# Performance work log

Hardware: AMD Instinct MI355X
Metric: run time of the kernel (lower is better)

The kernel has to match this reference:

```python
import jax, jax.numpy as jnp
import numpy as np

B, P_DIM, H_DIM, X_DIM = 4096, 1024, 2048, 1024


def setup_inputs() -> dict:
    key = jax.random.key(0)
    ks = jax.random.split(key, 24)
    def lin_w(k, out_d, in_d):
        bound = 1.0 / np.sqrt(in_d)
        return jax.random.uniform(k, (out_d, in_d), jnp.float32, -bound, bound)
    def lin_b(k, out_d, in_d):
        bound = 1.0 / np.sqrt(in_d)
        return jax.random.uniform(k, (out_d,), jnp.float32, -bound, bound)
    inp = {
        "P": jax.random.normal(ks[0], (B, P_DIM), jnp.float32),
        "hidden": jax.random.normal(ks[1], (B, H_DIM), jnp.float32),
        "cell": jax.random.normal(ks[2], (B, H_DIM), jnp.float32),
        "ext_input": jax.random.normal(ks[3], (B, X_DIM), jnp.float32),
        "W_pi": lin_w(ks[4], H_DIM, P_DIM), "b_pi": lin_b(ks[5], H_DIM, P_DIM),
        "W_pf": lin_w(ks[6], H_DIM, P_DIM), "b_pf": lin_b(ks[7], H_DIM, P_DIM),
        "W_pg": lin_w(ks[8], H_DIM, P_DIM), "b_pg": lin_b(ks[9], H_DIM, P_DIM),
        "W_po": lin_w(ks[10], H_DIM, P_DIM), "b_po": lin_b(ks[11], H_DIM, P_DIM),
        "W_hi": lin_w(ks[12], H_DIM, H_DIM), "W_hf": lin_w(ks[13], H_DIM, H_DIM),
        "W_hg": lin_w(ks[14], H_DIM, H_DIM), "W_ho": lin_w(ks[15], H_DIM, H_DIM),
        "W_xi": lin_w(ks[16], H_DIM, X_DIM), "W_xf": lin_w(ks[17], H_DIM, X_DIM),
        "W_xg": lin_w(ks[18], H_DIM, X_DIM), "W_xo": lin_w(ks[19], H_DIM, X_DIM),
    }
    return inp


def reference(P, hidden, cell, ext_input,
              W_pi, b_pi, W_pf, b_pf, W_pg, b_pg, W_po, b_po,
              W_hi, W_hf, W_hg, W_ho,
              W_xi, W_xf, W_xg, W_xo):
    # Concatenate the 4 per-gate weights along the output axis -> 3 big GEMMs
    # (mathematically identical to the 12 separate nn.Linear calls).
    Wp = jnp.concatenate([W_pi, W_pf, W_pg, W_po], axis=0)   # [4H, P]
    bp = jnp.concatenate([b_pi, b_pf, b_pg, b_po], axis=0)   # [4H]
    Wh = jnp.concatenate([W_hi, W_hf, W_hg, W_ho], axis=0)   # [4H, H]
    Wx = jnp.concatenate([W_xi, W_xf, W_xg, W_xo], axis=0)   # [4H, X]
    gates = P @ Wp.T + bp + hidden @ Wh.T + ext_input @ Wx.T  # [B, 4H]
    gi, gf, gg, go = jnp.split(gates, 4, axis=-1)
    i = jax.nn.sigmoid(gi)
    f = jax.nn.sigmoid(gf)
    g = jnp.tanh(gg)
    o = jax.nn.sigmoid(go)
    c_new = f * cell + i * g
    h_new = o * jnp.tanh(c_new)
    return (h_new, c_new)
```

## Files before the change

### kernel.cpp

```cpp
#include <hip/hip_runtime.h>
#include <hip/hip_bf16.h>
#include <stdint.h>

#define B_DIM 4096
#define P_DIMC 1024
#define H_DIMC 2048
#define X_DIMC 1024
#define K_DIM 4096
#define N_DIM 8192

#define BM 256
#define BN 256
#define BK 64
#define NT (K_DIM / BK)

typedef __attribute__((ext_vector_type(8))) short bf16x8;
typedef __attribute__((ext_vector_type(4))) float f32x4;

template <int V> struct Int { static constexpr int value = V; };

__device__ __forceinline__ unsigned short f2bf(float f) {
  union { float f; unsigned u; } v; v.f = f;
  unsigned u = v.u;
  u += 0x7FFFu + ((u >> 16) & 1u);
  return (unsigned short)(u >> 16);
}

__device__ __forceinline__ float sigm(float x) { return 1.f / (1.f + __expf(-x)); }
__device__ __forceinline__ float tanh_fast(float x) {
  float e = __expf(2.f * x);
  return 1.f - 2.f / (e + 1.f);
}

__device__ __forceinline__ void gl_lds16(const void* g, void* l) {
  __builtin_amdgcn_global_load_lds((const __attribute__((address_space(1))) void*)g,
                                   (__attribute__((address_space(3))) void*)l, 16, 0, 0);
}

struct WPtrs {
  const float *pi, *pf, *pg, *po;
  const float *hi, *hf, *hg, *ho;
  const float *xi, *xf, *xg, *xo;
};

__global__ void pack_kernel(const float* __restrict__ P, const float* __restrict__ Hd,
                            const float* __restrict__ X, WPtrs w,
                            unsigned short* __restrict__ A, unsigned short* __restrict__ Wo) {
  const int NA = B_DIM * (K_DIM / 8);
  const int NW = N_DIM * (K_DIM / 8);
  for (int idx = blockIdx.x * blockDim.x + threadIdx.x; idx < NA + NW;
       idx += gridDim.x * blockDim.x) {
    const float* src; int off; unsigned short* dst; size_t doff;
    if (idx < NA) {
      int row = idx >> 9;
      int col = (idx & 511) << 3;
      if (col < P_DIMC)                { src = P;  off = row * P_DIMC + col; }
      else if (col < P_DIMC + H_DIMC)  { src = Hd; off = row * H_DIMC + (col - P_DIMC); }
      else                             { src = X;  off = row * X_DIMC + (col - P_DIMC - H_DIMC); }
      dst = A; doff = (size_t)row * K_DIM + col;
    } else {
      int j = idx - NA;
      int n = j >> 9;
      int col = (j & 511) << 3;
      int gate = (n >> 4) & 3;
      int h = ((n >> 6) << 4) | (n & 15);
      if (col < P_DIMC) {
        src = gate == 0 ? w.pi : gate == 1 ? w.pf : gate == 2 ? w.pg : w.po;
        off = h * P_DIMC + col;
      } else if (col < P_DIMC + H_DIMC) {
        src = gate == 0 ? w.hi : gate == 1 ? w.hf : gate == 2 ? w.hg : w.ho;
        off = h * H_DIMC + (col - P_DIMC);
      } else {
        src = gate == 0 ? w.xi : gate == 1 ? w.xf : gate == 2 ? w.xg : w.xo;
        off = h * X_DIMC + (col - P_DIMC - H_DIMC);
      }
      dst = Wo; doff = (size_t)n * K_DIM + col;
    }
    float4 v0 = *(const float4*)(src + off);
    float4 v1 = *(const float4*)(src + off + 4);
    ushort4 o0, o1;
    o0.x = f2bf(v0.x); o0.y = f2bf(v0.y); o0.z = f2bf(v0.z); o0.w = f2bf(v0.w);
    o1.x = f2bf(v1.x); o1.y = f2bf(v1.y); o1.z = f2bf(v1.z); o1.w = f2bf(v1.w);
    union { ushort4 h[2]; uint4 u; } pk;
    pk.h[0] = o0; pk.h[1] = o1;
    *(uint4*)(dst + doff) = pk.u;
  }
}

__global__ __launch_bounds__(512, 1) void gemm_lstm_kernel(
    const unsigned short* __restrict__ A, const unsigned short* __restrict__ W,
    const float* __restrict__ cell,
    const float* __restrict__ bpi, const float* __restrict__ bpf,
    const float* __restrict__ bpg, const float* __restrict__ bpo,
    float* __restrict__ out) {
  __shared__ __align__(16) short As[2][BM * BK];
  __shared__ __align__(16) short Bs[2][BN * BK];

  const int T = threadIdx.x;
  const int wave = T >> 6, lane = T & 63;
  const int wm = wave >> 2, wn = wave & 3;

  const int x = blockIdx.x & 7, local = blockIdx.x >> 3;
  const int bm = (x & 1) * 8 + (local >> 3);
  const int bn = (x >> 1) * 8 + (local & 7);

  const int rowS = T >> 3;
  const int cg = ((T & 7) - (rowS & 7)) & 7;
  const unsigned short* aGq[4];
  const unsigned short* bGq[4];
#pragma unroll
  for (int q = 0; q < 4; ++q) {
    aGq[q] = A + (size_t)(bm * BM + q * 64 + rowS) * K_DIM + cg * 8;
    bGq[q] = W + (size_t)(bn * BN + q * 64 + rowS) * K_DIM + cg * 8;
  }
  const int dstOff = T * 8;

#define STAGE_TILE(BUF, KT)                                                   \
  _Pragma("unroll") for (int q = 0; q < 4; ++q)                               \
    gl_lds16(aGq[q] + (KT), &As[BUF][q * 4096] + dstOff);                     \
  _Pragma("unroll") for (int q = 0; q < 4; ++q)                               \
    gl_lds16(bGq[q] + (KT), &Bs[BUF][q * 4096] + dstOff);

  const int lrow = lane & 15, kgrp = lane >> 4;
  int offA[8][2], offB[4][2];
#pragma unroll
  for (int mf = 0; mf < 8; ++mf)
#pragma unroll
    for (int ks = 0; ks < 2; ++ks)
      offA[mf][ks] = (wm * 128 + mf * 16 + lrow) * BK +
                     (((ks * 4 + kgrp) + (lrow & 7)) & 7) * 8;
#pragma unroll
  for (int nf = 0; nf < 4; ++nf)
#pragma unroll
    for (int ks = 0; ks < 2; ++ks)
      offB[nf][ks] = (wn * 64 + nf * 16 + lrow) * BK +
                     (((ks * 4 + kgrp) + (lrow & 7)) & 7) * 8;

  f32x4 acc[8][4] = {};

  STAGE_TILE(0, 0)
  asm volatile("s_waitcnt vmcnt(0)" ::: "memory");
  __builtin_amdgcn_s_barrier();

  auto run_loop = [&](auto firstc) {
    constexpr int F = decltype(firstc)::value;
    constexpr int S = 4 - F;
    for (int t = 0; t < NT; ++t) {
      const int cur = t & 1, nxt = cur ^ 1;
      const short* bufA = &As[cur][0];
      const short* bufB = &Bs[cur][0];
      bf16x8 av[4], bv[4];

#pragma unroll
      for (int j = 0; j < 4; ++j) bv[j] = *(const bf16x8*)(bufB + offB[j][0]);
#pragma unroll
      for (int i = 0; i < 4; ++i) av[i] = *(const bf16x8*)(bufA + offA[F + i][0]);
      if (t < NT - 1) { STAGE_TILE(nxt, (t + 1) * BK) }
      __builtin_amdgcn_s_setprio(1);
#pragma unroll
      for (int mi = 0; mi < 4; ++mi)
#pragma unroll
        for (int ni = 0; ni < 4; ++ni)
          acc[F + mi][ni] =
              __builtin_amdgcn_mfma_f32_16x16x32_bf16(av[mi], bv[ni], acc[F + mi][ni], 0, 0, 0);
      __builtin_amdgcn_s_setprio(0);
      __builtin_amdgcn_sched_barrier(0);

#pragma unroll
      for (int i = 0; i < 4; ++i) av[i] = *(const bf16x8*)(bufA + offA[S + i][0]);
      __builtin_amdgcn_s_setprio(1);
#pragma unroll
      for (int mi = 0; mi < 4; ++mi)
#pragma unroll
        for (int ni = 0; ni < 4; ++ni)
          acc[S + mi][ni] =
              __builtin_amdgcn_mfma_f32_16x16x32_bf16(av[mi], bv[ni], acc[S + mi][ni], 0, 0, 0);
      __builtin_amdgcn_s_setprio(0);
      __builtin_amdgcn_sched_barrier(0);

#pragma unroll
      for (int j = 0; j < 4; ++j) bv[j] = *(const bf16x8*)(bufB + offB[j][1]);
#pragma unroll
      for (int i = 0; i < 4; ++i) av[i] = *(const bf16x8*)(bufA + offA[F + i][1]);
      __builtin_amdgcn_s_setprio(1);
#pragma unroll
      for (int mi = 0; mi < 4; ++mi)
#pragma unroll
        for (int ni = 0; ni < 4; ++ni)
          acc[F + mi][ni] =
              __builtin_amdgcn_mfma_f32_16x16x32_bf16(av[mi], bv[ni], acc[F + mi][ni], 0, 0, 0);
      __builtin_amdgcn_s_setprio(0);
      __builtin_amdgcn_sched_barrier(0);

#pragma unroll
      for (int i = 0; i < 4; ++i) av[i] = *(const bf16x8*)(bufA + offA[S + i][1]);
      __builtin_amdgcn_s_setprio(1);
#pragma unroll
      for (int mi = 0; mi < 4; ++mi)
#pragma unroll
        for (int ni = 0; ni < 4; ++ni)
          acc[S + mi][ni] =
              __builtin_amdgcn_mfma_f32_16x16x32_bf16(av[mi], bv[ni], acc[S + mi][ni], 0, 0, 0);
      __builtin_amdgcn_s_setprio(0);
      __builtin_amdgcn_sched_barrier(0);

      if (t < NT - 1) {
        asm volatile("s_waitcnt vmcnt(0)" ::: "memory");
        __builtin_amdgcn_s_barrier();
      }
    }
  };
  if (wave & 1) run_loop(Int<4>{});
  else          run_loop(Int<0>{});

  const int h = bn * 64 + wn * 16 + lrow;
  const float bi = bpi[h], bf_ = bpf[h], bg = bpg[h], bo = bpo[h];
  const int rbase = bm * BM + wm * 128 + kgrp * 4;
#pragma unroll
  for (int mf = 0; mf < 8; ++mf) {
#pragma unroll
    for (int r = 0; r < 4; ++r) {
      const int brow = rbase + mf * 16 + r;
      float gi = acc[mf][0][r] + bi;
      float gf = acc[mf][1][r] + bf_;
      float gg = acc[mf][2][r] + bg;
      float go = acc[mf][3][r] + bo;
      float i_ = sigm(gi), f_ = sigm(gf), g_ = tanh_fast(gg), o_ = sigm(go);
      float cold = cell[(size_t)brow * H_DIMC + h];
      float cn = f_ * cold + i_ * g_;
      out[(size_t)brow * H_DIMC + h] = o_ * tanh_fast(cn);
      out[(size_t)B_DIM * H_DIMC + (size_t)brow * H_DIMC + h] = cn;
    }
  }
}

extern "C" void kernel_launch(void* const* d_in, const int* in_sizes, int n_in,
                              void* d_out, int out_size, void* d_ws, size_t ws_size,
                              hipStream_t stream) {
  const float* P    = (const float*)d_in[0];
  const float* Hd   = (const float*)d_in[1];
  const float* cell = (const float*)d_in[2];
  const float* X    = (const float*)d_in[3];
  WPtrs w;
  w.pi = (const float*)d_in[4];   const float* bpi = (const float*)d_in[5];
  w.pf = (const float*)d_in[6];   const float* bpf = (const float*)d_in[7];
  w.pg = (const float*)d_in[8];   const float* bpg = (const float*)d_in[9];
  w.po = (const float*)d_in[10];  const float* bpo = (const float*)d_in[11];
  w.hi = (const float*)d_in[12];  w.hf = (const float*)d_in[13];
  w.hg = (const float*)d_in[14];  w.ho = (const float*)d_in[15];
  w.xi = (const float*)d_in[16];  w.xf = (const float*)d_in[17];
  w.xg = (const float*)d_in[18];  w.xo = (const float*)d_in[19];

  unsigned short* Abf = (unsigned short*)d_ws;
  unsigned short* Wbf = Abf + (size_t)B_DIM * K_DIM;

  pack_kernel<<<2048, 256, 0, stream>>>(P, Hd, X, w, Abf, Wbf);
  gemm_lstm_kernel<<<512, 512, 0, stream>>>(Abf, Wbf, cell, bpi, bpf, bpg, bpo,
                                            (float*)d_out);
}
```

Baseline: 302.6 us.

## Restructure GEMM main loop into half-tile ping-pong pipeline with interleaved weight layout

Splits each LDS buffer into two half-tiles and rewrites the main loop as an eight-phase schedule where each quarter of MFMA work is bracketed by barriers while the next half-tiles stream in, keeping more global loads in flight (vmcnt(6)) instead of draining to zero every K step. The weight permutation and the per-wave row/column mapping change so each wave owns interleaved 16-row/16-column slices, with the epilogue row indexing updated to match. The aim is better overlap of global-to-LDS traffic with matrix math. The cost is many more workgroup barriers per iteration and tighter coupling between waves.

```diff
diff --git a/kernel.cpp b/kernel.cpp
--- a/kernel.cpp
+++ b/kernel.cpp
@@ -62,8 +62,8 @@
       int j = idx - NA;
       int n = j >> 9;
       int col = (j & 511) << 3;
-      int gate = (n >> 4) & 3;
-      int h = ((n >> 6) << 4) | (n & 15);
+      int gate = (n >> 6) & 3;
+      int h = ((n >> 8) << 6) | (n & 63);
       if (col < P_DIMC) {
         src = gate == 0 ? w.pi : gate == 1 ? w.pf : gate == 2 ? w.pg : w.po;
         off = h * P_DIMC + col;
@@ -93,8 +93,8 @@
     const float* __restrict__ bpi, const float* __restrict__ bpf,
     const float* __restrict__ bpg, const float* __restrict__ bpo,
     float* __restrict__ out) {
-  __shared__ __align__(16) short As[2][BM * BK];
-  __shared__ __align__(16) short Bs[2][BN * BK];
+  __shared__ __align__(16) short As[2][2][8192];
+  __shared__ __align__(16) short Bs[2][2][8192];
 
   const int T = threadIdx.x;
   const int wave = T >> 6, lane = T & 63;
@@ -115,116 +115,122 @@
   }
   const int dstOff = T * 8;
 
-#define STAGE_TILE(BUF, KT)                                                   \
-  _Pragma("unroll") for (int q = 0; q < 4; ++q)                               \
-    gl_lds16(aGq[q] + (KT), &As[BUF][q * 4096] + dstOff);                     \
-  _Pragma("unroll") for (int q = 0; q < 4; ++q)                               \
-    gl_lds16(bGq[q] + (KT), &Bs[BUF][q * 4096] + dstOff);
+#define SA(BUF, HALF, KT)                                                     \
+  { gl_lds16(aGq[(HALF)*2] + (KT), &As[BUF][HALF][dstOff]);                   \
+    gl_lds16(aGq[(HALF)*2+1] + (KT), &As[BUF][HALF][4096 + dstOff]); }
+#define SB(BUF, HALF, KT)                                                     \
+  { gl_lds16(bGq[(HALF)*2] + (KT), &Bs[BUF][HALF][dstOff]);                   \
+    gl_lds16(bGq[(HALF)*2+1] + (KT), &Bs[BUF][HALF][4096 + dstOff]); }
 
   const int lrow = lane & 15, kgrp = lane >> 4;
-  int offA[8][2], offB[4][2];
-#pragma unroll
-  for (int mf = 0; mf < 8; ++mf)
+  int sl[2];
+#pragma unroll
+  for (int ks = 0; ks < 2; ++ks) sl[ks] = (((ks * 4 + kgrp) + (lrow & 7)) & 7) * 8;
+  int aOff[4][2], bOff[2][2];
+#pragma unroll
+  for (int i = 0; i < 4; ++i)
 #pragma unroll
     for (int ks = 0; ks < 2; ++ks)
-      offA[mf][ks] = (wm * 128 + mf * 16 + lrow) * BK +
-                     (((ks * 4 + kgrp) + (lrow & 7)) & 7) * 8;
-#pragma unroll
-  for (int nf = 0; nf < 4; ++nf)
+      aOff[i][ks] = (i * 32 + wm * 16 + lrow) * 64 + sl[ks];
+#pragma unroll
+  for (int j = 0; j < 2; ++j)
 #pragma unroll
     for (int ks = 0; ks < 2; ++ks)
-      offB[nf][ks] = (wn * 64 + nf * 16 + lrow) * BK +
-                     (((ks * 4 + kgrp) + (lrow & 7)) & 7) * 8;
+      bOff[j][ks] = (j * 64 + wn * 16 + lrow) * 64 + sl[ks];
 
   f32x4 acc[8][4] = {};
-
-  STAGE_TILE(0, 0)
-  asm volatile("s_waitcnt vmcnt(0)" ::: "memory");
-  __builtin_amdgcn_s_barrier();
-
-  auto run_loop = [&](auto firstc) {
-    constexpr int F = decltype(firstc)::value;
-    constexpr int S = 4 - F;
-    for (int t = 0; t < NT; ++t) {
-      const int cur = t & 1, nxt = cur ^ 1;
-      const short* bufA = &As[cur][0];
-      const short* bufB = &Bs[cur][0];
-      bf16x8 av[4], bv[4];
-
-#pragma unroll
-      for (int j = 0; j < 4; ++j) bv[j] = *(const bf16x8*)(bufB + offB[j][0]);
-#pragma unroll
-      for (int i = 0; i < 4; ++i) av[i] = *(const bf16x8*)(bufA + offA[F + i][0]);
-      if (t < NT - 1) { STAGE_TILE(nxt, (t + 1) * BK) }
-      __builtin_amdgcn_s_setprio(1);
-#pragma unroll
-      for (int mi = 0; mi < 4; ++mi)
-#pragma unroll
-        for (int ni = 0; ni < 4; ++ni)
-          acc[F + mi][ni] =
-              __builtin_amdgcn_mfma_f32_16x16x32_bf16(av[mi], bv[ni], acc[F + mi][ni], 0, 0, 0);
-      __builtin_amdgcn_s_setprio(0);
-      __builtin_amdgcn_sched_barrier(0);
-
-#pragma unroll
-      for (int i = 0; i < 4; ++i) av[i] = *(const bf16x8*)(bufA + offA[S + i][0]);
-      __builtin_amdgcn_s_setprio(1);
-#pragma unroll
-      for (int mi = 0; mi < 4; ++mi)
-#pragma unroll
-        for (int ni = 0; ni < 4; ++ni)
-          acc[S + mi][ni] =
-              __builtin_amdgcn_mfma_f32_16x16x32_bf16(av[mi], bv[ni], acc[S + mi][ni], 0, 0, 0);
-      __builtin_amdgcn_s_setprio(0);
-      __builtin_amdgcn_sched_barrier(0);
-
-#pragma unroll
-      for (int j = 0; j < 4; ++j) bv[j] = *(const bf16x8*)(bufB + offB[j][1]);
-#pragma unroll
-      for (int i = 0; i < 4; ++i) av[i] = *(const bf16x8*)(bufA + offA[F + i][1]);
-      __builtin_amdgcn_s_setprio(1);
-#pragma unroll
-      for (int mi = 0; mi < 4; ++mi)
-#pragma unroll
-        for (int ni = 0; ni < 4; ++ni)
-          acc[F + mi][ni] =
-              __builtin_amdgcn_mfma_f32_16x16x32_bf16(av[mi], bv[ni], acc[F + mi][ni], 0, 0, 0);
-      __builtin_amdgcn_s_setprio(0);
-      __builtin_amdgcn_sched_barrier(0);
-
-#pragma unroll
-      for (int i = 0; i < 4; ++i) av[i] = *(const bf16x8*)(bufA + offA[S + i][1]);
-      __builtin_amdgcn_s_setprio(1);
-#pragma unroll
-      for (int mi = 0; mi < 4; ++mi)
-#pragma unroll
-        for (int ni = 0; ni < 4; ++ni)
-          acc[S + mi][ni] =
-              __builtin_amdgcn_mfma_f32_16x16x32_bf16(av[mi], bv[ni], acc[S + mi][ni], 0, 0, 0);
-      __builtin_amdgcn_s_setprio(0);
-      __builtin_amdgcn_sched_barrier(0);
-
-      if (t < NT - 1) {
-        asm volatile("s_waitcnt vmcnt(0)" ::: "memory");
-        __builtin_amdgcn_s_barrier();
-      }
-    }
+  bf16x8 av[4][2], bv[2][2];
+
+#define RDA(BUF, HALF)                                                        \
+  _Pragma("unroll") for (int i = 0; i < 4; ++i) {                             \
+    av[i][0] = *(const bf16x8*)(&As[BUF][HALF][aOff[i][0]]);                  \
+    av[i][1] = *(const bf16x8*)(&As[BUF][HALF][aOff[i][1]]);                  \
+  }
+#define RDB(BUF, HALF)                                                        \
+  _Pragma("unroll") for (int j = 0; j < 2; ++j) {                             \
+    bv[j][0] = *(const bf16x8*)(&Bs[BUF][HALF][bOff[j][0]]);                  \
+    bv[j][1] = *(const bf16x8*)(&Bs[BUF][HALF][bOff[j][1]]);                  \
+  }
+#define FENCE()                                                               \
+  __builtin_amdgcn_s_barrier();                                               \
+  asm volatile("s_waitcnt lgkmcnt(0)" ::: "memory");                          \
+  __builtin_amdgcn_sched_barrier(0);
+#define MM(MH, NH)                                                            \
+  __builtin_amdgcn_s_setprio(1);                                              \
+  _Pragma("unroll") for (int i = 0; i < 4; ++i)                               \
+  _Pragma("unroll") for (int j = 0; j < 2; ++j) {                             \
+    acc[(MH)*4+i][(NH)*2+j] = __builtin_amdgcn_mfma_f32_16x16x32_bf16(        \
+        av[i][0], bv[j][0], acc[(MH)*4+i][(NH)*2+j], 0, 0, 0);                \
+    acc[(MH)*4+i][(NH)*2+j] = __builtin_amdgcn_mfma_f32_16x16x32_bf16(        \
+        av[i][1], bv[j][1], acc[(MH)*4+i][(NH)*2+j], 0, 0, 0);                \
+  }                                                                           \
+  __builtin_amdgcn_s_setprio(0);
+#define BAR() __builtin_amdgcn_s_barrier();
+
+  SA(0, 0, 0) SB(0, 0, 0) SA(0, 1, 0) SB(0, 1, 0)
+  SB(1, 0, BK) SA(1, 1, BK) SB(1, 1, BK)
+  asm volatile("s_waitcnt vmcnt(6)" ::: "memory");
+  BAR()
+
+  auto iter = [&](int t, auto lastc) {
+    constexpr bool LAST = decltype(lastc)::value;
+    const int k1 = (t + 1) * BK, k2 = (t + 2) * BK, k3 = (t + 3) * BK;
+    (void)k2; (void)k3;
+
+    RDA(0, 0) RDB(0, 0)
+    SA(1, 0, k1)
+    FENCE() MM(0, 0) BAR()
+    RDA(0, 1)
+    if constexpr (!LAST) SB(0, 0, k2)
+    FENCE() MM(1, 0) BAR()
+    RDB(0, 1)
+    if constexpr (!LAST) SA(0, 1, k2)
+    FENCE() MM(1, 1) BAR()
+    RDA(0, 0)
+    if constexpr (!LAST) SB(0, 1, k2)
+    FENCE() MM(0, 1)
+    if constexpr (!LAST) { asm volatile("s_waitcnt vmcnt(6)" ::: "memory"); }
+    else                 { asm volatile("s_waitcnt vmcnt(0)" ::: "memory"); }
+    BAR()
+    RDA(1, 0) RDB(1, 0)
+    if constexpr (!LAST) SA(0, 0, k2)
+    FENCE() MM(0, 0) BAR()
+    RDA(1, 1)
+    if constexpr (!LAST) SB(1, 0, k3)
+    FENCE() MM(1, 0) BAR()
+    RDB(1, 1)
+    if constexpr (!LAST) SA(1, 1, k3)
+    FENCE() MM(1, 1) BAR()
+    RDA(1, 0)
+    if constexpr (!LAST) SB(1, 1, k3)
+    FENCE() MM(0, 1)
+    if constexpr (!LAST) { asm volatile("s_waitcnt vmcnt(6)" ::: "memory"); }
+    BAR()
   };
-  if (wave & 1) run_loop(Int<4>{});
-  else          run_loop(Int<0>{});
+
+  for (int t = 0; t < NT - 2; t += 2) iter(t, Int<0>{});
+  iter(NT - 2, Int<1>{});
+
+#undef SA
+#undef SB
+#undef RDA
+#undef RDB
+#undef FENCE
+#undef MM
+#undef BAR
 
   const int h = bn * 64 + wn * 16 + lrow;
   const float bi = bpi[h], bf_ = bpf[h], bg = bpg[h], bo = bpo[h];
-  const int rbase = bm * BM + wm * 128 + kgrp * 4;
-#pragma unroll
-  for (int mf = 0; mf < 8; ++mf) {
+  const int rbase = bm * BM + wm * 16 + kgrp * 4;
+#pragma unroll
+  for (int a = 0; a < 8; ++a) {
 #pragma unroll
     for (int r = 0; r < 4; ++r) {
-      const int brow = rbase + mf * 16 + r;
-      float gi = acc[mf][0][r] + bi;
-      float gf = acc[mf][1][r] + bf_;
-      float gg = acc[mf][2][r] + bg;
-      float go = acc[mf][3][r] + bo;
+      const int brow = rbase + (a >> 2) * 128 + (a & 3) * 32 + r;
+      float gi = acc[a][0][r] + bi;
+      float gf = acc[a][1][r] + bf_;
+      float gg = acc[a][2][r] + bg;
+      float go = acc[a][3][r] + bo;
       float i_ = sigm(gi), f_ = sigm(gf), g_ = tanh_fast(gg), o_ = sigm(go);
       float cold = cell[(size_t)brow * H_DIMC + h];
       float cn = f_ * cold + i_ * g_;
```

Result: slower. 314.9 us (+4.1%).

## Switch GEMM to 32x32x16 MFMA with 4 waves and 128x128 warp tiles

Applied to the files above, without the earlier changes.

Replaces the 16x16x32 MFMA tiling (8 waves, 128x64 per wave) with 32x32x16 MFMA on 4 waves, each computing a 128x128 sub-tile. The weight pack interleave moves to 32-wide gate groups so each wave's four N-fragments line up with the i/f/g/o gates in the epilogue. LDS fragment reads are double-buffered in registers across the k-substeps. The goal is fewer LDS reads per MFMA and higher MFMA efficiency, at the cost of a large accumulator footprint (256 floats per lane) and half as many waves for hiding latency.

```diff
diff --git a/kernel.cpp b/kernel.cpp
--- a/kernel.cpp
+++ b/kernel.cpp
@@ -15,9 +15,7 @@
 #define NT (K_DIM / BK)
 
 typedef __attribute__((ext_vector_type(8))) short bf16x8;
-typedef __attribute__((ext_vector_type(4))) float f32x4;
-
-template <int V> struct Int { static constexpr int value = V; };
+typedef __attribute__((ext_vector_type(16))) float f32x16;
 
 __device__ __forceinline__ unsigned short f2bf(float f) {
   union { float f; unsigned u; } v; v.f = f;
@@ -62,8 +60,8 @@
       int j = idx - NA;
       int n = j >> 9;
       int col = (j & 511) << 3;
-      int gate = (n >> 4) & 3;
-      int h = ((n >> 6) << 4) | (n & 15);
+      int gate = (n >> 5) & 3;
+      int h = (n >> 7) * 32 + (n & 31);
       if (col < P_DIMC) {
         src = gate == 0 ? w.pi : gate == 1 ? w.pf : gate == 2 ? w.pg : w.po;
         off = h * P_DIMC + col;
@@ -87,7 +85,7 @@
   }
 }
 
-__global__ __launch_bounds__(512, 1) void gemm_lstm_kernel(
+__global__ __launch_bounds__(256, 1) void gemm_lstm_kernel(
     const unsigned short* __restrict__ A, const unsigned short* __restrict__ W,
     const float* __restrict__ cell,
     const float* __restrict__ bpi, const float* __restrict__ bpf,
@@ -98,7 +96,8 @@
 
   const int T = threadIdx.x;
   const int wave = T >> 6, lane = T & 63;
-  const int wm = wave >> 2, wn = wave & 3;
+  const int wm = wave >> 1, wn = wave & 1;
+  const int l31 = lane & 31, khalf = lane >> 5;
 
   const int x = blockIdx.x & 7, local = blockIdx.x >> 3;
   const int bm = (x & 1) * 8 + (local >> 3);
@@ -106,125 +105,89 @@
 
   const int rowS = T >> 3;
   const int cg = ((T & 7) - (rowS & 7)) & 7;
-  const unsigned short* aGq[4];
-  const unsigned short* bGq[4];
-#pragma unroll
-  for (int q = 0; q < 4; ++q) {
-    aGq[q] = A + (size_t)(bm * BM + q * 64 + rowS) * K_DIM + cg * 8;
-    bGq[q] = W + (size_t)(bn * BN + q * 64 + rowS) * K_DIM + cg * 8;
-  }
+  const unsigned short* aB = A + (size_t)(bm * BM + rowS) * K_DIM + cg * 8;
+  const unsigned short* bB = W + (size_t)(bn * BN + rowS) * K_DIM + cg * 8;
   const int dstOff = T * 8;
 
 #define STAGE_TILE(BUF, KT)                                                   \
-  _Pragma("unroll") for (int q = 0; q < 4; ++q)                               \
-    gl_lds16(aGq[q] + (KT), &As[BUF][q * 4096] + dstOff);                     \
-  _Pragma("unroll") for (int q = 0; q < 4; ++q)                               \
-    gl_lds16(bGq[q] + (KT), &Bs[BUF][q * 4096] + dstOff);
-
-  const int lrow = lane & 15, kgrp = lane >> 4;
-  int offA[8][2], offB[4][2];
-#pragma unroll
-  for (int mf = 0; mf < 8; ++mf)
-#pragma unroll
-    for (int ks = 0; ks < 2; ++ks)
-      offA[mf][ks] = (wm * 128 + mf * 16 + lrow) * BK +
-                     (((ks * 4 + kgrp) + (lrow & 7)) & 7) * 8;
-#pragma unroll
-  for (int nf = 0; nf < 4; ++nf)
-#pragma unroll
-    for (int ks = 0; ks < 2; ++ks)
-      offB[nf][ks] = (wn * 64 + nf * 16 + lrow) * BK +
-                     (((ks * 4 + kgrp) + (lrow & 7)) & 7) * 8;
-
-  f32x4 acc[8][4] = {};
+  _Pragma("unroll") for (int q = 0; q < 8; ++q)                               \
+    gl_lds16(aB + (size_t)q * 32 * K_DIM + (KT), &As[BUF][q * 2048] + dstOff);\
+  _Pragma("unroll") for (int q = 0; q < 8; ++q)                               \
+    gl_lds16(bB + (size_t)q * 32 * K_DIM + (KT), &Bs[BUF][q * 2048] + dstOff);
+
+  int sl[4];
+#pragma unroll
+  for (int ks = 0; ks < 4; ++ks)
+    sl[ks] = (((ks * 2 + khalf) + (l31 & 7)) & 7) * 8;
+  int offA[4][4], offB[4][4];
+#pragma unroll
+  for (int mf = 0; mf < 4; ++mf)
+#pragma unroll
+    for (int ks = 0; ks < 4; ++ks) {
+      offA[mf][ks] = (wm * 128 + mf * 32 + l31) * BK + sl[ks];
+      offB[mf][ks] = (wn * 128 + mf * 32 + l31) * BK + sl[ks];
+    }
+
+  f32x16 acc[4][4] = {};
+  bf16x8 av[2][4], bv[2][4];
 
   STAGE_TILE(0, 0)
   asm volatile("s_waitcnt vmcnt(0)" ::: "memory");
   __builtin_amdgcn_s_barrier();
 
-  auto run_loop = [&](auto firstc) {
-    constexpr int F = decltype(firstc)::value;
-    constexpr int S = 4 - F;
-    for (int t = 0; t < NT; ++t) {
-      const int cur = t & 1, nxt = cur ^ 1;
-      const short* bufA = &As[cur][0];
-      const short* bufB = &Bs[cur][0];
-      bf16x8 av[4], bv[4];
-
-#pragma unroll
-      for (int j = 0; j < 4; ++j) bv[j] = *(const bf16x8*)(bufB + offB[j][0]);
-#pragma unroll
-      for (int i = 0; i < 4; ++i) av[i] = *(const bf16x8*)(bufA + offA[F + i][0]);
-      if (t < NT - 1) { STAGE_TILE(nxt, (t + 1) * BK) }
+  for (int t = 0; t < NT; ++t) {
+    const int cur = t & 1, nxt = cur ^ 1;
+    const short* bufA = &As[cur][0];
+    const short* bufB = &Bs[cur][0];
+
+    if (t < NT - 1) { STAGE_TILE(nxt, (t + 1) * BK) }
+
+#pragma unroll
+    for (int i = 0; i < 4; ++i) {
+      av[0][i] = *(const bf16x8*)(bufA + offA[i][0]);
+      bv[0][i] = *(const bf16x8*)(bufB + offB[i][0]);
+    }
+    __builtin_amdgcn_sched_barrier(0);
+
+#pragma unroll
+    for (int ks = 0; ks < 4; ++ks) {
+      const int p = ks & 1, pn = p ^ 1;
+      if (ks < 3) {
+#pragma unroll
+        for (int i = 0; i < 4; ++i) {
+          av[pn][i] = *(const bf16x8*)(bufA + offA[i][ks + 1]);
+          bv[pn][i] = *(const bf16x8*)(bufB + offB[i][ks + 1]);
+        }
+      }
       __builtin_amdgcn_s_setprio(1);
 #pragma unroll
       for (int mi = 0; mi < 4; ++mi)
 #pragma unroll
         for (int ni = 0; ni < 4; ++ni)
-          acc[F + mi][ni] =
-              __builtin_amdgcn_mfma_f32_16x16x32_bf16(av[mi], bv[ni], acc[F + mi][ni], 0, 0, 0);
+          acc[mi][ni] = __builtin_amdgcn_mfma_f32_32x32x16_bf16(
+              av[p][mi], bv[p][ni], acc[mi][ni], 0, 0, 0);
       __builtin_amdgcn_s_setprio(0);
       __builtin_amdgcn_sched_barrier(0);
-
-#pragma unroll
-      for (int i = 0; i < 4; ++i) av[i] = *(const bf16x8*)(bufA + offA[S + i][0]);
-      __builtin_amdgcn_s_setprio(1);
-#pragma unroll
-      for (int mi = 0; mi < 4; ++mi)
-#pragma unroll
-        for (int ni = 0; ni < 4; ++ni)
-          acc[S + mi][ni] =
-              __builtin_amdgcn_mfma_f32_16x16x32_bf16(av[mi], bv[ni], acc[S + mi][ni], 0, 0, 0);
-      __builtin_amdgcn_s_setprio(0);
-      __builtin_amdgcn_sched_barrier(0);
-
-#pragma unroll
-      for (int j = 0; j < 4; ++j) bv[j] = *(const bf16x8*)(bufB + offB[j][1]);
-#pragma unroll
-      for (int i = 0; i < 4; ++i) av[i] = *(const bf16x8*)(bufA + offA[F + i][1]);
-      __builtin_amdgcn_s_setprio(1);
-#pragma unroll
-      for (int mi = 0; mi < 4; ++mi)
-#pragma unroll
-        for (int ni = 0; ni < 4; ++ni)
-          acc[F + mi][ni] =
-              __builtin_amdgcn_mfma_f32_16x16x32_bf16(av[mi], bv[ni], acc[F + mi][ni], 0, 0, 0);
-      __builtin_amdgcn_s_setprio(0);
-      __builtin_amdgcn_sched_barrier(0);
-
-#pragma unroll
-      for (int i = 0; i < 4; ++i) av[i] = *(const bf16x8*)(bufA + offA[S + i][1]);
-      __builtin_amdgcn_s_setprio(1);
-#pragma unroll
-      for (int mi = 0; mi < 4; ++mi)
-#pragma unroll
-        for (int ni = 0; ni < 4; ++ni)
-          acc[S + mi][ni] =
-              __builtin_amdgcn_mfma_f32_16x16x32_bf16(av[mi], bv[ni], acc[S + mi][ni], 0, 0, 0);
-      __builtin_amdgcn_s_setprio(0);
-      __builtin_amdgcn_sched_barrier(0);
-
-      if (t < NT - 1) {
-        asm volatile("s_waitcnt vmcnt(0)" ::: "memory");
-        __builtin_amdgcn_s_barrier();
-      }
-    }
-  };
-  if (wave & 1) run_loop(Int<4>{});
-  else          run_loop(Int<0>{});
-
-  const int h = bn * 64 + wn * 16 + lrow;
+    }
+
+    if (t < NT - 1) {
+      asm volatile("s_waitcnt vmcnt(0)" ::: "memory");
+      __builtin_amdgcn_s_barrier();
+    }
+  }
+
+  const int h = bn * 64 + wn * 32 + l31;
   const float bi = bpi[h], bf_ = bpf[h], bg = bpg[h], bo = bpo[h];
-  const int rbase = bm * BM + wm * 128 + kgrp * 4;
-#pragma unroll
-  for (int mf = 0; mf < 8; ++mf) {
-#pragma unroll
-    for (int r = 0; r < 4; ++r) {
-      const int brow = rbase + mf * 16 + r;
-      float gi = acc[mf][0][r] + bi;
-      float gf = acc[mf][1][r] + bf_;
-      float gg = acc[mf][2][r] + bg;
-      float go = acc[mf][3][r] + bo;
+  const int rbase = bm * BM + wm * 128 + khalf * 4;
+#pragma unroll
+  for (int mf = 0; mf < 4; ++mf) {
+#pragma unroll
+    for (int reg = 0; reg < 16; ++reg) {
+      const int brow = rbase + mf * 32 + (reg & 3) + 8 * (reg >> 2);
+      float gi = acc[mf][0][reg] + bi;
+      float gf = acc[mf][1][reg] + bf_;
+      float gg = acc[mf][2][reg] + bg;
+      float go = acc[mf][3][reg] + bo;
       float i_ = sigm(gi), f_ = sigm(gf), g_ = tanh_fast(gg), o_ = sigm(go);
       float cold = cell[(size_t)brow * H_DIMC + h];
       float cn = f_ * cold + i_ * g_;
@@ -255,6 +218,6 @@
   unsigned short* Wbf = Abf + (size_t)B_DIM * K_DIM;
 
   pack_kernel<<<2048, 256, 0, stream>>>(P, Hd, X, w, Abf, Wbf);
-  gemm_lstm_kernel<<<512, 512, 0, stream>>>(Abf, Wbf, cell, bpi, bpf, bpg, bpo,
+  gemm_lstm_kernel<<<512, 256, 0, stream>>>(Abf, Wbf, cell, bpi, bpf, bpg, bpo,
                                             (float*)d_out);
 }
```

Result: slower. 362.8 us (+19.9%).

## Use 4 waves per block with 128x128 per-wave tiles

Applied to the files above, without the earlier changes.

The GEMM block drops from 8 waves to 4. Each wave now computes a 128x128 output tile (8x8 MFMA fragments) instead of 128x64, which doubles register-level reuse of the A fragments and cuts LDS reads per MFMA. Global-to-LDS staging is redistributed so each of the 256 threads issues 8 loads per operand, and the epilogue loops over two gate groups. The cost is 256 accumulator floats per thread, with a risk of register spills, and fewer waves to hide latency.

```diff
diff --git a/kernel.cpp b/kernel.cpp
--- a/kernel.cpp
+++ b/kernel.cpp
@@ -87,7 +87,7 @@
   }
 }
 
-__global__ __launch_bounds__(512, 1) void gemm_lstm_kernel(
+__global__ __launch_bounds__(256, 1) void gemm_lstm_kernel(
     const unsigned short* __restrict__ A, const unsigned short* __restrict__ W,
     const float* __restrict__ cell,
     const float* __restrict__ bpi, const float* __restrict__ bpf,
@@ -98,7 +98,7 @@
 
   const int T = threadIdx.x;
   const int wave = T >> 6, lane = T & 63;
-  const int wm = wave >> 2, wn = wave & 3;
+  const int wm = wave >> 1, wn = wave & 1;
 
   const int x = blockIdx.x & 7, local = blockIdx.x >> 3;
   const int bm = (x & 1) * 8 + (local >> 3);
@@ -106,37 +106,28 @@
 
   const int rowS = T >> 3;
   const int cg = ((T & 7) - (rowS & 7)) & 7;
-  const unsigned short* aGq[4];
-  const unsigned short* bGq[4];
-#pragma unroll
-  for (int q = 0; q < 4; ++q) {
-    aGq[q] = A + (size_t)(bm * BM + q * 64 + rowS) * K_DIM + cg * 8;
-    bGq[q] = W + (size_t)(bn * BN + q * 64 + rowS) * K_DIM + cg * 8;
-  }
+  const unsigned short* aB = A + (size_t)(bm * BM + rowS) * K_DIM + cg * 8;
+  const unsigned short* bB = W + (size_t)(bn * BN + rowS) * K_DIM + cg * 8;
   const int dstOff = T * 8;
 
 #define STAGE_TILE(BUF, KT)                                                   \
-  _Pragma("unroll") for (int q = 0; q < 4; ++q)                               \
-    gl_lds16(aGq[q] + (KT), &As[BUF][q * 4096] + dstOff);                     \
-  _Pragma("unroll") for (int q = 0; q < 4; ++q)                               \
-    gl_lds16(bGq[q] + (KT), &Bs[BUF][q * 4096] + dstOff);
+  _Pragma("unroll") for (int q = 0; q < 8; ++q)                               \
+    gl_lds16(aB + (size_t)q * 32 * K_DIM + (KT), &As[BUF][q * 2048] + dstOff);\
+  _Pragma("unroll") for (int q = 0; q < 8; ++q)                               \
+    gl_lds16(bB + (size_t)q * 32 * K_DIM + (KT), &Bs[BUF][q * 2048] + dstOff);
 
   const int lrow = lane & 15, kgrp = lane >> 4;
-  int offA[8][2], offB[4][2];
+  int offA[8][2], offB[8][2];
 #pragma unroll
   for (int mf = 0; mf < 8; ++mf)
 #pragma unroll
-    for (int ks = 0; ks < 2; ++ks)
-      offA[mf][ks] = (wm * 128 + mf * 16 + lrow) * BK +
-                     (((ks * 4 + kgrp) + (lrow & 7)) & 7) * 8;
-#pragma unroll
-  for (int nf = 0; nf < 4; ++nf)
-#pragma unroll
-    for (int ks = 0; ks < 2; ++ks)
-      offB[nf][ks] = (wn * 64 + nf * 16 + lrow) * BK +
-                     (((ks * 4 + kgrp) + (lrow & 7)) & 7) * 8;
-
-  f32x4 acc[8][4] = {};
+    for (int ks = 0; ks < 2; ++ks) {
+      const int slot = (((ks * 4 + kgrp) + (lrow & 7)) & 7) * 8;
+      offA[mf][ks] = (wm * 128 + mf * 16 + lrow) * BK + slot;
+      offB[mf][ks] = (wn * 128 + mf * 16 + lrow) * BK + slot;
+    }
+
+  f32x4 acc[8][8] = {};
 
   STAGE_TILE(0, 0)
   asm volatile("s_waitcnt vmcnt(0)" ::: "memory");
@@ -149,10 +140,10 @@
       const int cur = t & 1, nxt = cur ^ 1;
       const short* bufA = &As[cur][0];
       const short* bufB = &Bs[cur][0];
-      bf16x8 av[4], bv[4];
-
-#pragma unroll
-      for (int j = 0; j < 4; ++j) bv[j] = *(const bf16x8*)(bufB + offB[j][0]);
+      bf16x8 av[4], bv[8];
+
+#pragma unroll
+      for (int j = 0; j < 8; ++j) bv[j] = *(const bf16x8*)(bufB + offB[j][0]);
 #pragma unroll
       for (int i = 0; i < 4; ++i) av[i] = *(const bf16x8*)(bufA + offA[F + i][0]);
       if (t < NT - 1) { STAGE_TILE(nxt, (t + 1) * BK) }
@@ -160,7 +151,7 @@
 #pragma unroll
       for (int mi = 0; mi < 4; ++mi)
 #pragma unroll
-        for (int ni = 0; ni < 4; ++ni)
+        for (int ni = 0; ni < 8; ++ni)
           acc[F + mi][ni] =
               __builtin_amdgcn_mfma_f32_16x16x32_bf16(av[mi], bv[ni], acc[F + mi][ni], 0, 0, 0);
       __builtin_amdgcn_s_setprio(0);
@@ -172,21 +163,21 @@
 #pragma unroll
       for (int mi = 0; mi < 4; ++mi)
 #pragma unroll
-        for (int ni = 0; ni < 4; ++ni)
+        for (int ni = 0; ni < 8; ++ni)
           acc[S + mi][ni] =
               __builtin_amdgcn_mfma_f32_16x16x32_bf16(av[mi], bv[ni], acc[S + mi][ni], 0, 0, 0);
       __builtin_amdgcn_s_setprio(0);
       __builtin_amdgcn_sched_barrier(0);
 
 #pragma unroll
-      for (int j = 0; j < 4; ++j) bv[j] = *(const bf16x8*)(bufB + offB[j][1]);
+      for (int j = 0; j < 8; ++j) bv[j] = *(const bf16x8*)(bufB + offB[j][1]);
 #pragma unroll
       for (int i = 0; i < 4; ++i) av[i] = *(const bf16x8*)(bufA + offA[F + i][1]);
       __builtin_amdgcn_s_setprio(1);
 #pragma unroll
       for (int mi = 0; mi < 4; ++mi)
 #pragma unroll
-        for (int ni = 0; ni < 4; ++ni)
+        for (int ni = 0; ni < 8; ++ni)
           acc[F + mi][ni] =
               __builtin_amdgcn_mfma_f32_16x16x32_bf16(av[mi], bv[ni], acc[F + mi][ni], 0, 0, 0);
       __builtin_amdgcn_s_setprio(0);
@@ -198,7 +189,7 @@
 #pragma unroll
       for (int mi = 0; mi < 4; ++mi)
 #pragma unroll
-        for (int ni = 0; ni < 4; ++ni)
+        for (int ni = 0; ni < 8; ++ni)
           acc[S + mi][ni] =
               __builtin_amdgcn_mfma_f32_16x16x32_bf16(av[mi], bv[ni], acc[S + mi][ni], 0, 0, 0);
       __builtin_amdgcn_s_setprio(0);
@@ -213,23 +204,26 @@
   if (wave & 1) run_loop(Int<4>{});
   else          run_loop(Int<0>{});
 
-  const int h = bn * 64 + wn * 16 + lrow;
-  const float bi = bpi[h], bf_ = bpf[h], bg = bpg[h], bo = bpo[h];
   const int rbase = bm * BM + wm * 128 + kgrp * 4;
 #pragma unroll
-  for (int mf = 0; mf < 8; ++mf) {
-#pragma unroll
-    for (int r = 0; r < 4; ++r) {
-      const int brow = rbase + mf * 16 + r;
-      float gi = acc[mf][0][r] + bi;
-      float gf = acc[mf][1][r] + bf_;
-      float gg = acc[mf][2][r] + bg;
-      float go = acc[mf][3][r] + bo;
-      float i_ = sigm(gi), f_ = sigm(gf), g_ = tanh_fast(gg), o_ = sigm(go);
-      float cold = cell[(size_t)brow * H_DIMC + h];
-      float cn = f_ * cold + i_ * g_;
-      out[(size_t)brow * H_DIMC + h] = o_ * tanh_fast(cn);
-      out[(size_t)B_DIM * H_DIMC + (size_t)brow * H_DIMC + h] = cn;
+  for (int hi2 = 0; hi2 < 2; ++hi2) {
+    const int h = (bn * 4 + wn * 2 + hi2) * 16 + lrow;
+    const float bi = bpi[h], bf_ = bpf[h], bg = bpg[h], bo = bpo[h];
+#pragma unroll
+    for (int mf = 0; mf < 8; ++mf) {
+#pragma unroll
+      for (int r = 0; r < 4; ++r) {
+        const int brow = rbase + mf * 16 + r;
+        float gi = acc[mf][hi2 * 4 + 0][r] + bi;
+        float gf = acc[mf][hi2 * 4 + 1][r] + bf_;
+        float gg = acc[mf][hi2 * 4 + 2][r] + bg;
+        float go = acc[mf][hi2 * 4 + 3][r] + bo;
+        float i_ = sigm(gi), f_ = sigm(gf), g_ = tanh_fast(gg), o_ = sigm(go);
+        float cold = cell[(size_t)brow * H_DIMC + h];
+        float cn = f_ * cold + i_ * g_;
+        out[(size_t)brow * H_DIMC + h] = o_ * tanh_fast(cn);
+        out[(size_t)B_DIM * H_DIMC + (size_t)brow * H_DIMC + h] = cn;
+      }
     }
   }
 }
@@ -255,6 +249,6 @@
   unsigned short* Wbf = Abf + (size_t)B_DIM * K_DIM;
 
   pack_kernel<<<2048, 256, 0, stream>>>(P, Hd, X, w, Abf, Wbf);
-  gemm_lstm_kernel<<<512, 512, 0, stream>>>(Abf, Wbf, cell, bpi, bpf, bpg, bpo,
+  gemm_lstm_kernel<<<512, 256, 0, stream>>>(Abf, Wbf, cell, bpi, bpf, bpg, bpo,
                                             (float*)d_out);
 }
```

After: 405.9 us. +34.2%, slower.
